# Kernel tuning notes

Measured on AMD Instinct MI355X. Metric: run time of the kernel, lower is better.

Reference implementation:

```python
import jax, jax.numpy as jnp
import numpy as np

KS = 3      # kernel_size
PAD = 1     # zero padding
N = KS * KS # sampling points per pixel
PI = 3.1415926


def conv2d(x, w, b=None, stride=1, padding=0):
    out = jax.lax.conv_general_dilated(
        x, w, (stride, stride), [(padding, padding), (padding, padding)],
        dimension_numbers=('NCHW', 'OIHW', 'NCHW'))
    if b is not None:
        out = out + b[None, :, None, None]
    return out


def setup_inputs() -> dict:
    key = jax.random.key(0)
    ks = jax.random.split(key, 8)
    B, C, OUTC, H, W = 4, 64, 64, 128, 128
    x = jax.random.normal(ks[0], (B, C, H, W), jnp.float32)
    w_b = jax.random.normal(ks[1], (OUTC, C, 3, 3), jnp.float32) * 0.05
    b_b = jax.random.normal(ks[2], (OUTC,), jnp.float32) * 0.05
    w_p = jax.random.normal(ks[3], (3, C, 3, 3), jnp.float32) * 0.05
    b_p = jax.random.normal(ks[4], (3,), jnp.float32) * 0.05
    w_m = jax.random.normal(ks[5], (N, C, 3, 3), jnp.float32) * 0.05
    b_m = jax.random.normal(ks[6], (N,), jnp.float32) * 0.05
    w_c = jax.random.normal(ks[7], (OUTC, C, 3, 3), jnp.float32) * 0.05
    return {"x": x, "w_b": w_b, "b_b": b_b, "w_p": w_p, "b_p": b_p,
            "w_m": w_m, "b_m": b_m, "w_c": w_c}


def reference(x, w_b, b_b, w_p, b_p, w_m, b_m, w_c):
    B, C, H, W = x.shape
    # bias branch: plain 3x3 conv, stride 1, pad 1
    bias = conv2d(x, w_b, b_b, stride=1, padding=1)
    # offset branch: conv -> sin -> (dropout eval = id) -> sigmoid
    off = jax.nn.sigmoid(jnp.sin(conv2d(x, w_p, b_p, stride=1, padding=1)))  # [B,3,H,W]
    l = off[:, 0] * 48.5 + 1.5          # [B,H,W] rect length
    wd = off[:, 1] * 48.5 + 1.5         # [B,H,W] rect width
    theta = off[:, 2] * PI              # [B,H,W] rotation angle
    # modulation mask
    m = jax.nn.sigmoid(conv2d(x, w_m, b_m, stride=1, padding=1))  # [B,9,H,W]

    # zero-pad input for sampling
    xp = jnp.pad(x, ((0, 0), (0, 0), (PAD, PAD), (PAD, PAD)))
    Hp, Wp = H + 2 * PAD, W + 2 * PAD

    # kernel grid offsets (ij meshgrid, x flattened first)
    rng = jnp.arange(-(KS - 1) // 2, (KS - 1) // 2 + 1, dtype=jnp.float32)
    pn_x = jnp.repeat(rng, KS)  # [N]  (-1,-1,-1,0,0,0,1,1,1)
    pn_y = jnp.tile(rng, KS)    # [N]  (-1,0,1,-1,0,1,-1,0,1)
    p0_x = jnp.arange(1, H + 1, dtype=jnp.float32)[:, None, None]  # [H,1,1]
    p0_y = jnp.arange(1, W + 1, dtype=jnp.float32)[None, :, None]  # [1,W,1]

    # sampling positions p = p0 + offset/3 * p_n, per point: [B,H,W,N]
    px = p0_x + (l[..., None] / 3.0) * pn_x
    py = p0_y + (wd[..., None] / 3.0) * pn_y
    ct = jnp.cos(theta)[..., None]  # [B,H,W,1]
    st = jnp.sin(theta)[..., None]
    pxx = px * ct - py * st
    pyy = px * st + py * ct

    # integer corners (non-diff, matches .detach().floor())
    fx = jnp.floor(jax.lax.stop_gradient(pxx))
    fy = jnp.floor(jax.lax.stop_gradient(pyy))
    qlt_x = jnp.clip(fx, 0, Hp - 1).astype(jnp.int32)
    qlt_y = jnp.clip(fy, 0, Wp - 1).astype(jnp.int32)
    qrb_x = jnp.clip(fx + 1, 0, Hp - 1).astype(jnp.int32)
    qrb_y = jnp.clip(fy + 1, 0, Wp - 1).astype(jnp.int32)

    # clamp continuous positions
    pcx = jnp.clip(pxx, 0, Hp - 1)
    pcy = jnp.clip(pyy, 0, Wp - 1)

    # bilinear weights
    g_lt = (1 + (qlt_x - pcx)) * (1 + (qlt_y - pcy))
    g_rb = (1 - (qrb_x - pcx)) * (1 - (qrb_y - pcy))
    g_lb = (1 + (qlt_x - pcx)) * (1 - (qrb_y - pcy))
    g_rt = (1 - (qrb_x - pcx)) * (1 + (qlt_y - pcy))

    # gather four corners: [B,C,H,W,N]
    def _gather_one(xp_b, qx_b, qy_b):
        return xp_b[:, qx_b, qy_b]  # [C,H,W,N]
    gather = jax.vmap(_gather_one)
    x_lt = gather(xp, qlt_x, qlt_y)
    x_rb = gather(xp, qrb_x, qrb_y)
    x_lb = gather(xp, qlt_x, qrb_y)
    x_rt = gather(xp, qrb_x, qlt_y)

    x_off = (g_lt[:, None] * x_lt + g_rb[:, None] * x_rb +
             g_lb[:, None] * x_lb + g_rt[:, None] * x_rt)  # [B,C,H,W,N]
    # modulation: [B,9,H,W] -> [B,1,H,W,9]
    x_off = x_off * jnp.transpose(m, (0, 2, 3, 1))[:, None]

    # rearrange [B,C,H,W,ks*ks] -> [B,C,H*ks,W*ks]
    x_off = x_off.reshape(B, C, H, W, KS, KS)
    x_off = jnp.transpose(x_off, (0, 1, 2, 4, 3, 5)).reshape(B, C, H * KS, W * KS)

    out = conv2d(x_off, w_c, None, stride=KS, padding=0) + bias
    return out
```

## Files before the change

kernel.cpp:

```cpp
#include <hip/hip_runtime.h>
#include <math.h>

#define BB 4
#define CC 64
#define OC 64
#define HH 128
#define WW 128
#define HP 130
#define WP 130
#define KTOT 1152
#define NKK 36
#define NKC 18
#define PIXT 32

#define XP_OFF 0
#define WR8_OFF 4326400
#define WPM8_OFF (4326400 + 36864)

typedef __attribute__((ext_vector_type(8))) short bf16x8;
typedef __attribute__((ext_vector_type(4))) short bf16x4;
typedef __attribute__((ext_vector_type(4))) float f32x4;

__device__ __forceinline__ float sigmoidf_(float z) {
    return 1.f / (1.f + expf(-z));
}
__device__ __forceinline__ unsigned short f2bf(float v) {
    union { float f; unsigned int u; } x; x.f = v;
    unsigned int r = x.u + 0x7FFF + ((x.u >> 16) & 1);
    return (unsigned short)(r >> 16);
}

#define NB_TR 1024
#define NB_BZ 516
#define NB_WR 288
#define NB_WPM 36

__global__ __launch_bounds__(256) void k_prep(
    const float* __restrict__ x,
    const float* __restrict__ w_b, const float* __restrict__ w_c,
    const float* __restrict__ w_p, const float* __restrict__ w_m,
    float* __restrict__ xp, unsigned short* __restrict__ wr8,
    unsigned short* __restrict__ wpm8)
{
    int bi = blockIdx.x;
    int tid = threadIdx.x;
    if (bi < NB_TR) {
        __shared__ float t[64][65];
        int b = bi >> 8;
        int h = (bi >> 1) & 127;
        int w0 = (bi & 1) * 64;
        int lane6 = tid & 63;
        for (int cc = tid >> 6; cc < 64; cc += 4)
            t[cc][lane6] = x[((b * 64 + cc) * 128 + h) * 128 + w0 + lane6];
        __syncthreads();
        for (int wsub = tid >> 6; wsub < 64; wsub += 4)
            xp[((size_t)(b * HP + h + 1) * WP + (w0 + wsub + 1)) * 64 + lane6] = t[lane6][wsub];
        return;
    }
    bi -= NB_TR;
    if (bi < NB_BZ) {
        int idx = bi * 256 + tid;
        int c = idx & 63;
        int tt = idx >> 6;
        int b = tt / 516;
        int j = tt % 516;
        int hp, wp;
        if (j < 130)      { hp = 0;       wp = j; }
        else if (j < 260) { hp = 129;     wp = j - 130; }
        else if (j < 388) { hp = j - 259; wp = 0; }
        else              { hp = j - 387; wp = 129; }
        xp[((size_t)(b * HP + hp) * WP + wp) * 64 + c] = 0.f;
        return;
    }
    bi -= NB_BZ;
    if (bi < NB_WR) {
        int idx = bi * 256 + tid;
        int j    = idx & 7;
        int lane = (idx >> 3) & 63;
        int ot   = (idx >> 9) & 3;
        int kk   = idx >> 11;
        int o  = ot * 16 + (lane & 15);
        int k  = kk * 32 + (lane >> 4) * 8 + j;
        int slot = k >> 6;
        int c    = k & 63;
        float v;
        if (slot < 9) v = w_b[((o * CC + c) * 3 + slot / 3) * 3 + slot % 3];
        else { int n = slot - 9; v = w_c[((o * CC + c) * 3 + n / 3) * 3 + n % 3]; }
        wr8[idx] = f2bf(v);
        return;
    }
    bi -= NB_WR;
    {
        int idx = bi * 256 + tid;
        if (idx >= NKC * 64 * 8) return;
        int j    = idx & 7;
        int lane = (idx >> 3) & 63;
        int kk   = idx >> 9;
        int ch = lane & 15;
        int k  = kk * 32 + (lane >> 4) * 8 + j;
        int tap = k >> 6;
        int c   = k & 63;
        float v = 0.f;
        if (ch < 3)       v = w_p[((ch * CC + c) * 3 + tap / 3) * 3 + tap % 3];
        else if (ch < 12) v = w_m[(((ch - 3) * CC + c) * 3 + tap / 3) * 3 + tap % 3];
        wpm8[idx] = f2bf(v);
    }
}

__global__ __launch_bounds__(512, 4) void k_main(
    const float* __restrict__ xp, const unsigned short* __restrict__ wr8,
    const unsigned short* __restrict__ wpm8,
    const float* __restrict__ w_p,
    const float* __restrict__ b_p, const float* __restrict__ b_m,
    const float* __restrict__ b_b, float* __restrict__ out)
{
    __shared__ unsigned short U8[2 * 18432];
    __shared__ float wth[16][9][4];

    int tid = threadIdx.x;
    int lane = tid & 63;
    int g = tid >> 6;
    int p_sub = lane >> 4;
    int cq = lane & 15;
    int c0 = cq * 4;

    int bid = blockIdx.x;
    int swz = (bid & 7) * 256 + (bid >> 3);
    int pixBase = swz * PIXT;

    for (int i = tid; i < 576; i += 512) {
        int cqi = i / 36;
        int rest = i % 36;
        int tap = rest >> 2;
        int e = rest & 3;
        int c = cqi * 4 + e;
        wth[cqi][tap][e] = w_p[((2 * CC + c) * 3 + tap / 3) * 3 + tap % 3];
    }
    __syncthreads();

    int p_local = g * 4 + p_sub;
    int ph = p_local >> 4;
    int p16 = p_local & 15;
    int pix = pixBase + p_local;
    int b = pix >> 14;
    int h = (pix >> 7) & 127;
    int w = pix & 127;
    const float* xb = xp + (size_t)b * HP * WP * 64;

    float th = 0.f;
#pragma unroll
    for (int tap = 0; tap < 9; ++tap) {
        int ti = tap / 3, tj = tap % 3;
        float4 xv = *(const float4*)&xb[((h + ti) * WP + (w + tj)) * 64 + c0];
        float4 wt = *(const float4*)&wth[cq][tap][0];
        th += xv.x * wt.x + xv.y * wt.y + xv.z * wt.z + xv.w * wt.w;
        int k = tap * 64 + c0;
        int kqt = k >> 3;
        int blk = kqt * 16 + (p16 ^ (kqt & 15));
        bf16x4 pk;
        pk[0] = (short)f2bf(xv.x); pk[1] = (short)f2bf(xv.y);
        pk[2] = (short)f2bf(xv.z); pk[3] = (short)f2bf(xv.w);
        *(bf16x4*)&U8[ph * 18432 + blk * 8 + (k & 7)] = pk;
    }
    th += __shfl_xor(th, 1);
    th += __shfl_xor(th, 2);
    th += __shfl_xor(th, 4);
    th += __shfl_xor(th, 8);
    __syncthreads();

    int kq = lane >> 4;
    f32x4 ca = {0.f, 0.f, 0.f, 0.f}, cb = {0.f, 0.f, 0.f, 0.f};
    {
        int colp = lane & 3;
        int pabs = g * 4 + colp;
        int phc = g >> 2;
        int p16c = pabs & 15;
        const bf16x8* av = (const bf16x8*)wpm8;
#pragma unroll
        for (int kk = 0; kk < NKC; ++kk) {
            bf16x8 a = av[kk * 64 + lane];
            int kqt = kk * 4 + kq;
            int blk = kqt * 16 + (p16c ^ (kqt & 15));
            bf16x8 bf = *(const bf16x8*)&U8[phc * 18432 + blk * 8];
            if (kk & 1) cb = __builtin_amdgcn_mfma_f32_16x16x32_bf16(a, bf, cb, 0, 0, 0);
            else        ca = __builtin_amdgcn_mfma_f32_16x16x32_bf16(a, bf, ca, 0, 0, 0);
        }
        ca[0] += cb[0]; ca[1] += cb[1]; ca[2] += cb[2]; ca[3] += cb[3];
    }
    float conv[12];
#pragma unroll
    for (int ch = 0; ch < 12; ++ch) {
        conv[ch] = __shfl(ca[ch & 3], ((ch >> 2) << 4) + p_sub);
    }

    float l  = sigmoidf_(sinf(conv[0] + b_p[0])) * 48.5f + 1.5f;
    float wd = sigmoidf_(sinf(conv[1] + b_p[1])) * 48.5f + 1.5f;
    float theta = sigmoidf_(sinf(th + b_p[2])) * 3.1415926f;
    float ct = cosf(theta), st = sinf(theta);
    float px0 = (float)(h + 1);
    float py0 = (float)(w + 1);

#pragma unroll
    for (int n = 0; n < 9; ++n) {
        float mm = sigmoidf_(conv[3 + n] + b_m[n]);
        float pnx = (float)(n / 3 - 1);
        float pny = (float)(n % 3 - 1);
        float px = px0 + (l * (1.f / 3.f)) * pnx;
        float py = py0 + (wd * (1.f / 3.f)) * pny;
        float pxx = px * ct - py * st;
        float pyy = px * st + py * ct;
        float fx = floorf(pxx);
        float fy = floorf(pyy);
        int qltx = min(max((int)fx, 0), HP - 1);
        int qlty = min(max((int)fy, 0), WP - 1);
        int qrbx = min(max((int)fx + 1, 0), HP - 1);
        int qrby = min(max((int)fy + 1, 0), WP - 1);
        float pcx = fminf(fmaxf(pxx, 0.f), (float)(HP - 1));
        float pcy = fminf(fmaxf(pyy, 0.f), (float)(WP - 1));
        float dltx = 1.f + ((float)qltx - pcx);
        float drbx = 1.f - ((float)qrbx - pcx);
        float dlty = 1.f + ((float)qlty - pcy);
        float drby = 1.f - ((float)qrby - pcy);
        float g_lt = dltx * dlty * mm;
        float g_rb = drbx * drby * mm;
        float g_lb = dltx * drby * mm;
        float g_rt = drbx * dlty * mm;
        float4 xlt = *(const float4*)&xb[(qltx * WP + qlty) * 64 + c0];
        float4 xrb = *(const float4*)&xb[(qrbx * WP + qrby) * 64 + c0];
        float4 xlb = *(const float4*)&xb[(qltx * WP + qrby) * 64 + c0];
        float4 xrt = *(const float4*)&xb[(qrbx * WP + qlty) * 64 + c0];
        float v0 = g_lt * xlt.x + g_rb * xrb.x + g_lb * xlb.x + g_rt * xrt.x;
        float v1 = g_lt * xlt.y + g_rb * xrb.y + g_lb * xlb.y + g_rt * xrt.y;
        float v2 = g_lt * xlt.z + g_rb * xrb.z + g_lb * xlb.z + g_rt * xrt.z;
        float v3 = g_lt * xlt.w + g_rb * xrb.w + g_lb * xlb.w + g_rt * xrt.w;
        int k = (9 + n) * 64 + c0;
        int kqt = k >> 3;
        int blk = kqt * 16 + (p16 ^ (kqt & 15));
        bf16x4 pk;
        pk[0] = (short)f2bf(v0); pk[1] = (short)f2bf(v1);
        pk[2] = (short)f2bf(v2); pk[3] = (short)f2bf(v3);
        *(bf16x4*)&U8[ph * 18432 + blk * 8 + (k & 7)] = pk;
    }
    __syncthreads();

    int ot = g & 3;
    int ph2 = g >> 2;
    int pn = lane & 15;
    f32x4 a0 = {0.f, 0.f, 0.f, 0.f}, a1 = {0.f, 0.f, 0.f, 0.f};
    const bf16x8* wv = (const bf16x8*)wr8;
#pragma unroll
    for (int kk = 0; kk < NKK; ++kk) {
        bf16x8 a = wv[(kk * 4 + ot) * 64 + lane];
        int kqt = kk * 4 + kq;
        int blk = kqt * 16 + (pn ^ (kqt & 15));
        bf16x8 bf = *(const bf16x8*)&U8[ph2 * 18432 + blk * 8];
        if (kk & 1) a1 = __builtin_amdgcn_mfma_f32_16x16x32_bf16(a, bf, a1, 0, 0, 0);
        else        a0 = __builtin_amdgcn_mfma_f32_16x16x32_bf16(a, bf, a0, 0, 0, 0);
    }

    int pix2 = pixBase + ph2 * 16 + pn;
    int bb2 = pix2 >> 14;
    int hw = pix2 & 16383;
#pragma unroll
    for (int r2 = 0; r2 < 4; ++r2) {
        int o = ot * 16 + kq * 4 + r2;
        out[((size_t)(bb2 * 64 + o)) * 16384 + hw] = a0[r2] + a1[r2] + b_b[o];
    }
}

extern "C" void kernel_launch(void* const* d_in, const int* in_sizes, int n_in,
                              void* d_out, int out_size, void* d_ws, size_t ws_size,
                              hipStream_t stream) {
    const float* x   = (const float*)d_in[0];
    const float* w_b = (const float*)d_in[1];
    const float* b_b = (const float*)d_in[2];
    const float* w_p = (const float*)d_in[3];
    const float* b_p = (const float*)d_in[4];
    const float* w_m = (const float*)d_in[5];
    const float* b_m = (const float*)d_in[6];
    const float* w_c = (const float*)d_in[7];
    float* out = (float*)d_out;

    float* ws = (float*)d_ws;
    float* xp = ws + XP_OFF;
    unsigned short* wr8  = (unsigned short*)(ws + WR8_OFF);
    unsigned short* wpm8 = (unsigned short*)(ws + WPM8_OFF);

    k_prep<<<NB_TR + NB_BZ + NB_WR + NB_WPM, 256, 0, stream>>>(
        x, w_b, w_c, w_p, w_m, xp, wr8, wpm8);
    k_main<<<(BB * HH * WW) / PIXT, 512, 0, stream>>>(
        xp, wr8, wpm8, w_p, b_p, b_m, b_b, out);
}
```

Measured before the change: 79.55 us.

## Distribute per-pixel offset math across lanes and use fast transcendental intrinsics

Each lane in a 16-lane group previously computed all nine sampling positions, bilinear weights and sigmoid/sin/cos for its pixel redundantly. Now each lane computes one sampling point (or one of l/wd/cos/sin) and the results are broadcast to the group with shuffles, packing the four corner indices into one 32-bit word. Transcendentals are also replaced by hardware exp2/rcp/sin/cos intrinsics with range reduction via fract. This cuts redundant ALU work but adds many cross-lane shuffles and lowers accuracy of sin/cos/exp.

```diff
diff --git a/kernel.cpp b/kernel.cpp
--- a/kernel.cpp
+++ b/kernel.cpp
@@ -21,13 +21,27 @@
 typedef __attribute__((ext_vector_type(4))) short bf16x4;
 typedef __attribute__((ext_vector_type(4))) float f32x4;
 
-__device__ __forceinline__ float sigmoidf_(float z) {
-    return 1.f / (1.f + expf(-z));
-}
 __device__ __forceinline__ unsigned short f2bf(float v) {
     union { float f; unsigned int u; } x; x.f = v;
     unsigned int r = x.u + 0x7FFF + ((x.u >> 16) & 1);
     return (unsigned short)(r >> 16);
+}
+
+__device__ __forceinline__ float fexp_(float x) {
+    return __builtin_amdgcn_exp2f(x * 1.44269504089f);
+}
+__device__ __forceinline__ float fsig_(float z) {
+    return __builtin_amdgcn_rcpf(1.f + fexp_(-z));
+}
+__device__ __forceinline__ float fsin_(float x) {
+    float r = x * 0.15915494309f;
+    r = __builtin_amdgcn_fractf(r);
+    return __builtin_amdgcn_sinf(r);
+}
+__device__ __forceinline__ float fcos_(float x) {
+    float r = x * 0.15915494309f;
+    r = __builtin_amdgcn_fractf(r);
+    return __builtin_amdgcn_cosf(r);
 }
 
 #define NB_TR 1024
@@ -187,26 +201,38 @@
         }
         ca[0] += cb[0]; ca[1] += cb[1]; ca[2] += cb[2]; ca[3] += cb[3];
     }
-    float conv[12];
-#pragma unroll
-    for (int ch = 0; ch < 12; ++ch) {
-        conv[ch] = __shfl(ca[ch & 3], ((ch >> 2) << 4) + p_sub);
-    }
-
-    float l  = sigmoidf_(sinf(conv[0] + b_p[0])) * 48.5f + 1.5f;
-    float wd = sigmoidf_(sinf(conv[1] + b_p[1])) * 48.5f + 1.5f;
-    float theta = sigmoidf_(sinf(th + b_p[2])) * 3.1415926f;
-    float ct = cosf(theta), st = sinf(theta);
-    float px0 = (float)(h + 1);
-    float py0 = (float)(w + 1);
-
-#pragma unroll
-    for (int n = 0; n < 9; ++n) {
-        float mm = sigmoidf_(conv[3 + n] + b_m[n]);
+
+    int base16 = p_sub << 4;
+    int chc = (cq < 9) ? (3 + cq) : 3;
+    int srcL = ((chc >> 2) << 4) + p_sub;
+    float m0 = __shfl(ca[0], srcL);
+    float m1 = __shfl(ca[1], srcL);
+    float m2 = __shfl(ca[2], srcL);
+    float m3 = __shfl(ca[3], srcL);
+    int jj = chc & 3;
+    float cm = (jj == 0) ? m0 : (jj == 1) ? m1 : (jj == 2) ? m2 : m3;
+    float c0v = __shfl(ca[0], p_sub);
+    float c1v = __shfl(ca[1], p_sub);
+
+    float bp0 = b_p[0], bp1 = b_p[1], bp2 = b_p[2];
+    float hval = 0.f;
+    if (cq == 9)       hval = fsig_(fsin_(c0v + bp0)) * 48.5f + 1.5f;
+    else if (cq == 10) hval = fsig_(fsin_(c1v + bp1)) * 48.5f + 1.5f;
+    else if (cq == 11) hval = fcos_(fsig_(fsin_(th + bp2)) * 3.1415926f);
+    else if (cq == 12) hval = fsin_(fsig_(fsin_(th + bp2)) * 3.1415926f);
+    float l  = __shfl(hval, base16 + 9);
+    float wd = __shfl(hval, base16 + 10);
+    float ct = __shfl(hval, base16 + 11);
+    float st = __shfl(hval, base16 + 12);
+
+    unsigned int qpack; float glt, grb, glb, grt;
+    {
+        int n = (cq < 9) ? cq : 8;
+        float mm = fsig_(cm + b_m[n]);
         float pnx = (float)(n / 3 - 1);
         float pny = (float)(n % 3 - 1);
-        float px = px0 + (l * (1.f / 3.f)) * pnx;
-        float py = py0 + (wd * (1.f / 3.f)) * pny;
+        float px = (float)(h + 1) + (l * (1.f / 3.f)) * pnx;
+        float py = (float)(w + 1) + (wd * (1.f / 3.f)) * pny;
         float pxx = px * ct - py * st;
         float pyy = px * st + py * ct;
         float fx = floorf(pxx);
@@ -221,10 +247,23 @@
         float drbx = 1.f - ((float)qrbx - pcx);
         float dlty = 1.f + ((float)qlty - pcy);
         float drby = 1.f - ((float)qrby - pcy);
-        float g_lt = dltx * dlty * mm;
-        float g_rb = drbx * drby * mm;
-        float g_lb = dltx * drby * mm;
-        float g_rt = drbx * dlty * mm;
+        glt = dltx * dlty * mm;
+        grb = drbx * drby * mm;
+        glb = dltx * drby * mm;
+        grt = drbx * dlty * mm;
+        qpack = (unsigned)qltx | ((unsigned)qlty << 8) |
+                ((unsigned)qrbx << 16) | ((unsigned)qrby << 24);
+    }
+
+#pragma unroll
+    for (int n = 0; n < 9; ++n) {
+        unsigned int q = __shfl(qpack, base16 + n);
+        float g_lt = __shfl(glt, base16 + n);
+        float g_rb = __shfl(grb, base16 + n);
+        float g_lb = __shfl(glb, base16 + n);
+        float g_rt = __shfl(grt, base16 + n);
+        int qltx = q & 255, qlty = (q >> 8) & 255;
+        int qrbx = (q >> 16) & 255, qrby = (q >> 24) & 255;
         float4 xlt = *(const float4*)&xb[(qltx * WP + qlty) * 64 + c0];
         float4 xrb = *(const float4*)&xb[(qrbx * WP + qrby) * 64 + c0];
         float4 xlb = *(const float4*)&xb[(qltx * WP + qrby) * 64 + c0];
```

Result: faster. 71.75 us (-9.8%).
